# Performance work log

Measured on AMD Instinct MI355X. Metric: run time of the kernel, lower is better.

The kernel has to match this reference:

```python
import jax, jax.numpy as jnp
import numpy as np
from math import factorial

IRREPS = [0] * 256 + [1] * 256 + [2] * 128 + [3] * 64
N_BATCH, CHANNELS = 1024, 32


def _dfact(n):
    r = 1
    while n > 1:
        r *= n
        n -= 2
    return r


def _sh_l(l, xyz):
    """Real spherical harmonics of degree l, components m=-l..l, at unit vectors xyz."""
    x, y, z = xyz[:, 0], xyz[:, 1], xyz[:, 2]
    phi = np.arctan2(y, x)
    ct = z
    st = np.sqrt(np.clip(1.0 - ct * ct, 0.0, None))
    Y = np.zeros((xyz.shape[0], 2 * l + 1))
    for m in range(l + 1):
        pmm = ((-1.0) ** m) * _dfact(2 * m - 1) * st ** m  # P_m^m(cos t)
        if l == m:
            plm = pmm
        else:
            pm1 = ct * (2 * m + 1) * pmm  # P_{m+1}^m
            if l == m + 1:
                plm = pm1
            else:
                p2, p1 = pmm, pm1
                for ll in range(m + 2, l + 1):
                    p2, p1 = p1, ((2 * ll - 1) * ct * p1 - (ll + m - 1) * p2) / (ll - m)
                plm = p1
        K = np.sqrt((2 * l + 1) / (4 * np.pi) * factorial(l - m) / factorial(l + m))
        if m == 0:
            Y[:, l] = K * plm
        else:
            Y[:, l + m] = np.sqrt(2.0) * K * np.cos(m * phi) * plm
            Y[:, l - m] = np.sqrt(2.0) * K * np.sin(m * phi) * plm
    return Y


def _j_matrix(l):
    """Orthogonal involution J_l: real-SH matrix of the y<->z axis swap (J = J^T = J^-1)."""
    rng = np.random.default_rng(0)
    v = rng.normal(size=(max(256, 16 * (2 * l + 1)), 3))
    v /= np.linalg.norm(v, axis=1, keepdims=True)
    A = _sh_l(l, v)
    B = _sh_l(l, v[:, [0, 2, 1]])  # Y(swap r)
    X, _, _, _ = np.linalg.lstsq(A, B, rcond=None)
    return X.T  # Y(swap r) = J @ Y(r)


def _build_info():
    freq, rev, groups = [], [], []
    off = 0
    i = 0
    while i < len(IRREPS):
        l = IRREPS[i]
        mul = 0
        while i < len(IRREPS) and IRREPS[i] == l:
            mul += 1
            i += 1
        d = 2 * l + 1
        groups.append((l, off, mul, np.asarray(_j_matrix(l), np.float32)))
        for _ in range(mul):
            for k in range(d):
                freq.append(k - l)      # m value of component k
                rev.append(off + (d - 1 - k))  # index of the -m partner
            off += d
    return np.asarray(freq, np.float32), np.asarray(rev, np.int32), groups, off


FREQ_NP, REV_NP, GROUPS, DIM = _build_info()
FREQ = jnp.asarray(FREQ_NP)
REV = jnp.asarray(REV_NP)
J_MATS = [jnp.asarray(J) for (_, _, _, J) in GROUPS]


def _z_rot(x, theta):
    """Per-m z-rotation (sparse vecsca): out_m = cos(m t) x_m - sin(m t) x_{-m}."""
    ang = theta[:, None] * FREQ  # (N, DIM)
    return jnp.cos(ang)[..., None] * x - jnp.sin(ang)[..., None] * x[:, REV, :]


def _j_apply(x):
    """Block-diagonal J application, grouped by l (sparse scale / flip stage)."""
    n, _, c = x.shape
    outs = []
    for (l, off, mul, _), J in zip(GROUPS, J_MATS):
        d = 2 * l + 1
        seg = x[:, off:off + mul * d, :].reshape(n, mul, d, c)
        outs.append(jnp.einsum('pq,nmqc->nmpc', J, seg).reshape(n, mul * d, c))
    return jnp.concatenate(outs, axis=1)


def setup_inputs() -> dict:
    key = jax.random.key(0)
    k0, k1, k2, k3 = jax.random.split(key, 4)
    two_pi = 2.0 * np.pi
    return {
        'input': jax.random.normal(k0, (N_BATCH, DIM, CHANNELS), dtype=jnp.float32),
        'alpha': jax.random.uniform(k1, (N_BATCH,), dtype=jnp.float32) * two_pi,
        'beta': jax.random.uniform(k2, (N_BATCH,), dtype=jnp.float32) * two_pi,
        'gamma': jax.random.uniform(k3, (N_BATCH,), dtype=jnp.float32) * two_pi,
    }


def reference(input, alpha, beta, gamma):
    # D(alpha, beta, gamma) = Dz(alpha) J Dz(beta) J Dz(gamma)
    x = _z_rot(input, gamma)
    x = _j_apply(x)
    x = _z_rot(x, beta)
    x = _j_apply(x)
    return _z_rot(x, alpha)
```

## Files before the change

### kernel.cpp

```cpp
#include <hip/hip_runtime.h>
#include <math.h>


namespace {

typedef float f4 __attribute__((ext_vector_type(4)));

constexpr float SQ3_2 = 0.86602540378443864676f;
constexpr float S6    = 0.61237243569579452455f;
constexpr float S10   = 0.79056941504209483300f;
constexpr float S15   = 0.96824583655185422129f;

template<int L> struct JM;
template<> struct JM<1> {
  static constexpr float v[3][3] = {
    { 0.f, -1.f, 0.f},
    {-1.f,  0.f, 0.f},
    { 0.f,  0.f, 1.f}};
};
template<> struct JM<2> {
  static constexpr float v[5][5] = {
    { 0.f, 0.f,  0.f,   -1.f,  0.f},
    { 0.f, 1.f,  0.f,    0.f,  0.f},
    { 0.f, 0.f, -0.5f,   0.f, -SQ3_2},
    {-1.f, 0.f,  0.f,    0.f,  0.f},
    { 0.f, 0.f, -SQ3_2,  0.f,  0.5f}};
};
template<> struct JM<3> {
  static constexpr float v[7][7] = {
    { 0.f, 0.f, 0.f, S10,  0.f,   -S6,  0.f},
    { 0.f, 1.f, 0.f, 0.f,  0.f,    0.f, 0.f},
    { 0.f, 0.f, 0.f, S6,   0.f,    S10, 0.f},
    { S10, 0.f, S6,  0.f,  0.f,    0.f, 0.f},
    { 0.f, 0.f, 0.f, 0.f, -0.25f,  0.f, -S15},
    {-S6,  0.f, S10, 0.f,  0.f,    0.f, 0.f},
    { 0.f, 0.f, 0.f, 0.f, -S15,    0.f, 0.25f}};
};

template<int L>
__device__ inline void compute_M_col(int q, float al, float be, float ga, float* M) {
  constexpr int D = 2 * L + 1;
  const int mq = q - L;
  float sg, cg;
  sincosf((float)mq * ga, &sg, &cg);
  float v[D];
#pragma unroll
  for (int p = 0; p < D; ++p)
    v[p] = cg * JM<L>::v[p][q] + sg * JM<L>::v[p][(D - 1) - q];
  float c1, s1;
  sincosf(be, &s1, &c1);
  float cb[L + 1], sb[L + 1];
  cb[0] = 1.f; sb[0] = 0.f;
  cb[1] = c1;  sb[1] = s1;
#pragma unroll
  for (int k = 2; k <= L; ++k) {
    cb[k] = 2.f * c1 * cb[k - 1] - cb[k - 2];
    sb[k] = 2.f * c1 * sb[k - 1] - sb[k - 2];
  }
  float w[D];
#pragma unroll
  for (int p = 0; p < D; ++p) {
    const int mp = p - L;
    const int am = mp < 0 ? -mp : mp;
    const float c = cb[am];
    const float s = mp < 0 ? -sb[am] : sb[am];
    w[p] = c * v[p] - s * v[(D - 1) - p];
  }
  float u[D];
#pragma unroll
  for (int p = 0; p < D; ++p) {
    float acc = 0.f;
#pragma unroll
    for (int r = 0; r < D; ++r) acc = fmaf(JM<L>::v[p][r], w[r], acc);
    u[p] = acc;
  }
  sincosf(al, &s1, &c1);
  float ca[L + 1], sa[L + 1];
  ca[0] = 1.f; sa[0] = 0.f;
  ca[1] = c1;  sa[1] = s1;
#pragma unroll
  for (int k = 2; k <= L; ++k) {
    ca[k] = 2.f * c1 * ca[k - 1] - ca[k - 2];
    sa[k] = 2.f * c1 * sa[k - 1] - sa[k - 2];
  }
#pragma unroll
  for (int p = 0; p < D; ++p) {
    const int mp = p - L;
    const int am = mp < 0 ? -mp : mp;
    const float c = ca[am];
    const float s = mp < 0 ? -sa[am] : sa[am];
    M[p * D + q] = c * u[p] - s * u[(D - 1) - p];
  }
}

__global__ __launch_bounds__(256) void build_M_kernel(
    const float* __restrict__ alpha, const float* __restrict__ beta,
    const float* __restrict__ gamma, float* __restrict__ ws, int n_batch) {
  const int t = threadIdx.x;
  const int n = blockIdx.x * 16 + (t >> 4);
  const int col = t & 15;
  if (n >= n_batch || col >= 15) return;
  const float al = alpha[n], be = beta[n], ga = gamma[n];
  float* w = ws + (size_t)n * 96;
  if (col < 7)       compute_M_col<3>(col,      al, be, ga, w);
  else if (col < 12) compute_M_col<2>(col - 7,  al, be, ga, w + 49);
  else               compute_M_col<1>(col - 12, al, be, ga, w + 74);
}

__device__ inline void gload16(const void* g, void* l) {
  __builtin_amdgcn_global_load_lds(
      (const __attribute__((address_space(1))) void*)g,
      (__attribute__((address_space(3))) void*)l, 16, 0, 0);
}

template<int D, int CHUNK_ROWS, int NCHUNK>
__device__ inline void apply_section(const f4* __restrict__ inSec,
                                     f4* __restrict__ outSec,
                                     const float* __restrict__ M,
                                     f4* __restrict__ buf, int t) {
  constexpr int F = CHUNK_ROWS * 8;
  constexpr int ITER = (F + 511) / 512;
  for (int c = 0; c < NCHUNK; ++c) {
    const f4* src = inSec + c * F;
#pragma unroll
    for (int i = 0; i < ITER; ++i) {
      const int k = t + 512 * i;
      if (k < F) gload16(src + k, buf + k);
    }
    __syncthreads();
    f4* dst = outSec + c * F;
#pragma unroll
    for (int i = 0; i < ITER; ++i) {
      const int k = t + 512 * i;
      if (k < F) {
        const int r = k >> 3;
        const int p = r % D;
        const float* Mrow = M + p * D;
        const f4* b = buf + (k - p * 8);
        f4 a = Mrow[0] * b[0];
#pragma unroll
        for (int q = 1; q < D; ++q) a += Mrow[q] * b[q * 8];
        dst[k] = a;
      }
    }
    __syncthreads();
  }
}

__global__ __launch_bounds__(512, 4) void wigner_stream_kernel(
    const float* __restrict__ in, const float* __restrict__ ws,
    float* __restrict__ out) {
  __shared__ f4 buf[1792];
  __shared__ float M[96];
  const int n = blockIdx.x;
  const int t = threadIdx.x;
  if (t < 83) M[t] = ws[(size_t)n * 96 + t];

  const size_t base = (size_t)n * (2112 * 8);
  const f4* inN = (const f4*)in + base;
  f4* outN = (f4*)out + base;

#pragma unroll
  for (int i = 0; i < 4; ++i) outN[t + 512 * i] = inN[t + 512 * i];

  apply_section<3, 192, 4>(inN + 256 * 8, outN + 256 * 8, M + 74, buf, t);
  apply_section<5, 160, 4>(inN + 1024 * 8, outN + 1024 * 8, M + 49, buf, t);
  apply_section<7, 224, 2>(inN + 1664 * 8, outN + 1664 * 8, M, buf, t);
}

}

extern "C" void kernel_launch(void* const* d_in, const int* in_sizes, int n_in,
                              void* d_out, int out_size, void* d_ws, size_t ws_size,
                              hipStream_t stream) {
  const float* in    = (const float*)d_in[0];
  const float* alpha = (const float*)d_in[1];
  const float* beta  = (const float*)d_in[2];
  const float* gamma = (const float*)d_in[3];
  float* out = (float*)d_out;
  const int n_batch = in_sizes[1];

  float* ws = (float*)d_ws;
  build_M_kernel<<<(n_batch + 15) / 16, 256, 0, stream>>>(alpha, beta, gamma,
                                                          ws, n_batch);
  wigner_stream_kernel<<<n_batch, 512, 0, stream>>>(in, ws, out);
}
```

Baseline: 120.9 us.

## Replace LDS-staged chunks with direct global reads and split each batch across two blocks

Drops the global_load_lds staging buffer and the per-chunk barriers. Each output element now reads its D input rows straight from global memory and relies on cache for reuse across the rows of an irrep block. The grid doubles, with two blocks per batch element: one handles the l=0/l=1 part and the other handles l=2/l=3. This is meant to raise parallelism and remove sync stalls. The costs are redundant global/L2 reads (each input row is fetched D times) and uneven work between the two halves.

```diff
diff --git a/kernel.cpp b/kernel.cpp
--- a/kernel.cpp
+++ b/kernel.cpp
@@ -107,65 +107,56 @@
   else               compute_M_col<1>(col - 12, al, be, ga, w + 74);
 }
 
-__device__ inline void gload16(const void* g, void* l) {
-  __builtin_amdgcn_global_load_lds(
-      (const __attribute__((address_space(1))) void*)g,
-      (__attribute__((address_space(3))) void*)l, 16, 0, 0);
+template<int D>
+__device__ inline f4 apply_elem(const f4* __restrict__ inN,
+                                const float* __restrict__ M,
+                                int r, int off, int ch) {
+  const int p = (r - off) % D;
+  const float* Mrow = M + p * D;
+  const f4* b = inN + (r - p) * 8 + ch;
+  f4 a = Mrow[0] * b[0];
+#pragma unroll
+  for (int q = 1; q < D; ++q) a += Mrow[q] * b[q * 8];
+  return a;
 }
 
-template<int D, int CHUNK_ROWS, int NCHUNK>
-__device__ inline void apply_section(const f4* __restrict__ inSec,
-                                     f4* __restrict__ outSec,
-                                     const float* __restrict__ M,
-                                     f4* __restrict__ buf, int t) {
-  constexpr int F = CHUNK_ROWS * 8;
-  constexpr int ITER = (F + 511) / 512;
-  for (int c = 0; c < NCHUNK; ++c) {
-    const f4* src = inSec + c * F;
-#pragma unroll
-    for (int i = 0; i < ITER; ++i) {
-      const int k = t + 512 * i;
-      if (k < F) gload16(src + k, buf + k);
-    }
-    __syncthreads();
-    f4* dst = outSec + c * F;
-#pragma unroll
-    for (int i = 0; i < ITER; ++i) {
-      const int k = t + 512 * i;
-      if (k < F) {
-        const int r = k >> 3;
-        const int p = r % D;
-        const float* Mrow = M + p * D;
-        const f4* b = buf + (k - p * 8);
-        f4 a = Mrow[0] * b[0];
-#pragma unroll
-        for (int q = 1; q < D; ++q) a += Mrow[q] * b[q * 8];
-        dst[k] = a;
-      }
-    }
-    __syncthreads();
-  }
-}
-
-__global__ __launch_bounds__(512, 4) void wigner_stream_kernel(
+__global__ __launch_bounds__(512) void wigner_stream_kernel(
     const float* __restrict__ in, const float* __restrict__ ws,
     float* __restrict__ out) {
-  __shared__ f4 buf[1792];
   __shared__ float M[96];
-  const int n = blockIdx.x;
+  const int bid = blockIdx.x;
+  const int n = bid >> 1;
+  const int half = bid & 1;
   const int t = threadIdx.x;
   if (t < 83) M[t] = ws[(size_t)n * 96 + t];
+  __syncthreads();
 
-  const size_t base = (size_t)n * (2112 * 8);
+  const size_t base = (size_t)n * 16896;
   const f4* inN = (const f4*)in + base;
   f4* outN = (f4*)out + base;
+  const int g = t >> 3;
+  const int ch = t & 7;
 
+  if (half == 0) {
 #pragma unroll
-  for (int i = 0; i < 4; ++i) outN[t + 512 * i] = inN[t + 512 * i];
-
-  apply_section<3, 192, 4>(inN + 256 * 8, outN + 256 * 8, M + 74, buf, t);
-  apply_section<5, 160, 4>(inN + 1024 * 8, outN + 1024 * 8, M + 49, buf, t);
-  apply_section<7, 224, 2>(inN + 1664 * 8, outN + 1664 * 8, M, buf, t);
+    for (int i = 0; i < 4; ++i) outN[512 * i + t] = inN[512 * i + t];
+#pragma unroll
+    for (int i = 4; i < 16; ++i) {
+      const int r = 64 * i + g;
+      outN[512 * i + t] = apply_elem<3>(inN, M + 74, r, 256, ch);
+    }
+  } else {
+#pragma unroll
+    for (int i = 16; i < 26; ++i) {
+      const int r = 64 * i + g;
+      outN[512 * i + t] = apply_elem<5>(inN, M + 49, r, 1024, ch);
+    }
+#pragma unroll
+    for (int i = 26; i < 33; ++i) {
+      const int r = 64 * i + g;
+      outN[512 * i + t] = apply_elem<7>(inN, M, r, 1664, ch);
+    }
+  }
 }
 
 }
@@ -183,5 +174,5 @@
   float* ws = (float*)d_ws;
   build_M_kernel<<<(n_batch + 15) / 16, 256, 0, stream>>>(alpha, beta, gamma,
                                                           ws, n_batch);
-  wigner_stream_kernel<<<n_batch, 512, 0, stream>>>(in, ws, out);
+  wigner_stream_kernel<<<n_batch * 2, 512, 0, stream>>>(in, ws, out);
 }
```

After: 136.5 us. +12.9%, slower.
